# Optimization experiments

Hardware: AMD Instinct MI355X
Metric: run time of the kernel (lower is better)

The kernel has to match this reference:

```python
import jax, jax.numpy as jnp
import numpy as np

NUM_HEAD = 16
D_MODEL = 1024


def setup_inputs() -> dict:
    key = jax.random.key(0)
    ks = jax.random.split(key, 11)
    B, S, D = 2, 2048, D_MODEL
    scale = 1.0 / np.sqrt(D)
    inp = {
        "q": jax.random.normal(ks[0], (B, S, D), dtype=jnp.float32),
        "k": jax.random.normal(ks[1], (B, S, D), dtype=jnp.float32),
        "v": jax.random.normal(ks[2], (B, S, D), dtype=jnp.float32),
        "Wq": jax.random.normal(ks[3], (D, D), dtype=jnp.float32) * scale,
        "bq": jnp.zeros((D,), dtype=jnp.float32),
        "Wk": jax.random.normal(ks[4], (D, D), dtype=jnp.float32) * scale,
        "bk": jnp.zeros((D,), dtype=jnp.float32),
        "Wv": jax.random.normal(ks[5], (D, D), dtype=jnp.float32) * scale,
        "bv": jnp.zeros((D,), dtype=jnp.float32),
        "Wo": jax.random.normal(ks[6], (D, D), dtype=jnp.float32) * scale,
        "bo": jnp.zeros((D,), dtype=jnp.float32),
    }
    return inp


def _split_heads(x, num_head):
    B, S, D = x.shape
    return x.reshape(B, S, num_head, D // num_head).transpose(0, 2, 1, 3)  # [B,H,S,d]


def reference(q, k, v, Wq, bq, Wk, bk, Wv, bv, Wo, bo):
    H = NUM_HEAD
    qp = q @ Wq + bq
    kp = k @ Wk + bk  # computed but UNUSED, matching source bug
    vp = v @ Wv + bv
    # source bug: k := split_heads(v-projection)
    qh = _split_heads(qp, H)          # [B,H,S,d]
    kh = _split_heads(vp, H)          # [B,H,S,d]  (v-projection used as keys)
    vh = _split_heads(vp, H)          # [B,H,S,d]
    d = qh.shape[-1]
    scores = jnp.einsum('bhqd,bhkd->bhqk', qh, kh) / jnp.sqrt(jnp.asarray(d, qh.dtype))
    attn = jax.nn.softmax(scores, axis=-1)
    out = jnp.einsum('bhqk,bhkd->bhqd', attn, vh)  # [B,H,S,d]
    B, _, S, _ = out.shape
    out = out.transpose(0, 2, 1, 3).reshape(B, S, H * d)
    return out @ Wo + bo
```

## Files before the change

### kernel.cpp

```cpp
#include <hip/hip_runtime.h>
#include <hip/hip_bf16.h>

using bfrag  = __attribute__((ext_vector_type(8))) __bf16;
using f32x4  = __attribute__((ext_vector_type(4))) float;
using f32x16 = __attribute__((ext_vector_type(16))) float;
using v4u    = __attribute__((ext_vector_type(4))) unsigned int;
using v2u    = __attribute__((ext_vector_type(2))) unsigned int;

__device__ __forceinline__ ushort f2bf(float f) {
    union { float f; unsigned u; } c; c.f = f;
    return (ushort)((c.u + 0x7fffu + ((c.u >> 16) & 1u)) >> 16);
}

__device__ __forceinline__ unsigned pack_bf16x2(float lo, float hi) {
    union { __hip_bfloat162 h; unsigned u; } c;
    c.h = __float22bfloat162_rn(make_float2(lo, hi));
    return c.u;
}

__device__ __forceinline__ void gld_lds16(const ushort* g, ushort* l) {
    __builtin_amdgcn_global_load_lds(
        (const __attribute__((address_space(1))) void*)g,
        (__attribute__((address_space(3))) void*)l, 16, 0, 0);
}

__device__ __forceinline__ f32x16 mfma32(bfrag a, bfrag b, f32x16 c) {
    return __builtin_amdgcn_mfma_f32_32x32x16_bf16(a, b, c, 0, 0, 0);
}


__global__ void cvt_bf16_2(const float* __restrict__ a, ushort* __restrict__ da,
                           const float* __restrict__ b, ushort* __restrict__ db, int n4) {
    int i = blockIdx.x * blockDim.x + threadIdx.x;
    const float* s; ushort* d;
    if (i < n4) { s = a; d = da; } else { s = b; d = db; i -= n4; }
    float4 f = ((const float4*)s)[i];
    ((ushort4*)d)[i] = make_ushort4(f2bf(f.x), f2bf(f.y), f2bf(f.z), f2bf(f.w));
}

__global__ void cvt_T3(const float* __restrict__ s0, ushort* __restrict__ d0,
                       const float* __restrict__ s1, ushort* __restrict__ d1,
                       const float* __restrict__ s2, ushort* __restrict__ d2) {
    __shared__ float t[32][33];
    const int z = blockIdx.z;
    const float* src = z == 0 ? s0 : z == 1 ? s1 : s2;
    ushort* dst = z == 0 ? d0 : z == 1 ? d1 : d2;
    const int tx = threadIdx.x, ty = threadIdx.y;
    const int c0 = blockIdx.x * 32, r0 = blockIdx.y * 32;
    for (int i = ty; i < 32; i += 8) t[i][tx] = src[(size_t)(r0 + i) * 1024 + c0 + tx];
    __syncthreads();
    for (int i = ty; i < 32; i += 8) dst[(size_t)(c0 + i) * 1024 + r0 + tx] = f2bf(t[tx][i]);
}


__global__ __launch_bounds__(256) void vpt_T(const ushort* __restrict__ VPb, ushort* __restrict__ VPT) {
    __shared__ ushort T[64][72];
    const int st = blockIdx.x, bh = blockIdx.y;
    const int b = bh >> 4, h = bh & 15;
    const int tid = threadIdx.x;
#pragma unroll
    for (int i = 0; i < 2; ++i) {
        const int c = tid + i * 256;
        const int row = c >> 3, col8 = (c & 7) * 8;
        v4u d = *(const v4u*)(VPb + (size_t)(b * 2048 + st * 64 + row) * 1024 + h * 64 + col8);
        *(v4u*)&T[row][col8] = d;
    }
    __syncthreads();
    const int d = tid >> 2, sch = tid & 3;
    union { ushort s[16]; v4u v[2]; } tmp;
#pragma unroll
    for (int j = 0; j < 16; ++j) {
        const int js = (j & 3) | ((j >> 1) & 4) | ((j << 1) & 8);
        tmp.s[j] = T[sch * 16 + js][d];
    }
    ushort* dst = VPT + ((size_t)bh * 64 + d) * 2048 + st * 64 + sch * 16;
    *(v4u*)dst = tmp.v[0];
    *(v4u*)(dst + 8) = tmp.v[1];
}


template<bool BF16OUT>
__device__ __forceinline__ void gemm_body(
    const ushort* __restrict__ A, const ushort* __restrict__ Bt,
    const float* __restrict__ bias, void* __restrict__ Cout,
    float scale, int bM, int bN)
{
    __shared__ ushort As[2][128 * 32];
    __shared__ ushort Bs[2][128 * 32];
    const int tid = threadIdx.x;
    const int lane = tid & 63, w = tid >> 6;
    const int l15 = lane & 15, lg = lane >> 4;
    const int wr = w >> 1, wc = w & 1;

    const ushort* Ag = A + (size_t)bM * 128 * 1024;
    const ushort* Bg = Bt + (size_t)bN * 128 * 1024;
    const int r0 = w * 32 + (lane >> 2);
    const int cc = (lane & 3) * 8;

    auto STAGE = [&](int buf, int kt) {
        const int kk = kt * 32;
#pragma unroll
        for (int i = 0; i < 2; ++i) {
            const int row = r0 + i * 16;
            const int c = w * 2 + i;
            gld_lds16(Ag + (size_t)row * 1024 + kk + cc, &As[buf][c * 512]);
            gld_lds16(Bg + (size_t)row * 1024 + kk + cc, &Bs[buf][c * 512]);
        }
    };

    f32x4 acc[4][4];
#pragma unroll
    for (int m = 0; m < 4; ++m)
#pragma unroll
        for (int n = 0; n < 4; ++n) acc[m][n] = (f32x4){0.f, 0.f, 0.f, 0.f};

    STAGE(0, 0);
    __syncthreads();
    int cur = 0;
    for (int kt = 0; kt < 32; ++kt) {
        if (kt < 31) STAGE(cur ^ 1, kt + 1);
        bfrag aF[4], bF[4];
#pragma unroll
        for (int m = 0; m < 4; ++m) aF[m] = *(const bfrag*)&As[cur][(wr * 64 + m * 16 + l15) * 32 + lg * 8];
#pragma unroll
        for (int n = 0; n < 4; ++n) bF[n] = *(const bfrag*)&Bs[cur][(wc * 64 + n * 16 + l15) * 32 + lg * 8];
        __builtin_amdgcn_s_setprio(1);
#pragma unroll
        for (int m = 0; m < 4; ++m)
#pragma unroll
            for (int n = 0; n < 4; ++n)
                acc[m][n] = __builtin_amdgcn_mfma_f32_16x16x32_bf16(aF[m], bF[n], acc[m][n], 0, 0, 0);
        __builtin_amdgcn_s_setprio(0);
        if (kt < 31) {
            __syncthreads();
            cur ^= 1;
        }
    }

#pragma unroll
    for (int m = 0; m < 4; ++m)
#pragma unroll
        for (int n = 0; n < 4; ++n) {
            const int gcol = bN * 128 + wc * 64 + n * 16 + l15;
            const float bv = bias[gcol];
#pragma unroll
            for (int j = 0; j < 4; ++j) {
                const int grow = bM * 128 + wr * 64 + m * 16 + lg * 4 + j;
                const float val = (acc[m][n][j] + bv) * scale;
                if constexpr (BF16OUT) {
                    ((ushort*)Cout)[(size_t)grow * 1024 + gcol] = f2bf(val);
                } else {
                    ((float*)Cout)[(size_t)grow * 1024 + gcol] = val;
                }
            }
        }
}

__global__ __launch_bounds__(256) void gemm_qv(
    const ushort* __restrict__ Aq, const ushort* __restrict__ Wq, const float* __restrict__ bq, ushort* __restrict__ Cq,
    const ushort* __restrict__ Av, const ushort* __restrict__ Wv, const float* __restrict__ bv, ushort* __restrict__ Cv,
    float qscale)
{
    const int z = blockIdx.z;
    gemm_body<true>(z ? Av : Aq, z ? Wv : Wq, z ? bv : bq, z ? (void*)Cv : (void*)Cq,
                    z ? 1.0f : qscale, blockIdx.y, blockIdx.x);
}

__global__ __launch_bounds__(256) void gemm_o(
    const ushort* __restrict__ A, const ushort* __restrict__ Bt,
    const float* __restrict__ bias, float* __restrict__ Cout)
{
    gemm_body<false>(A, Bt, bias, Cout, 1.0f, blockIdx.y, blockIdx.x);
}


__global__ __launch_bounds__(512, 2) void attn_kernel(
    const ushort* __restrict__ QP, const ushort* __restrict__ VP,
    const ushort* __restrict__ VPT, ushort* __restrict__ AO)
{
    __shared__ ushort Ks[3][4096];
    __shared__ ushort Vs[2][4096];
    const int tid = threadIdx.x;
    const int w = tid >> 6, lane = tid & 63;
    const int l31 = lane & 31, hi = lane >> 5;
    const int bh = blockIdx.x, qt = blockIdx.y;
    const int b = bh >> 4, h = bh & 15;
    const int qrow0 = qt * 256 + w * 32;

    const int r_st = tid >> 3;
    const int sc = ((tid & 7) ^ (r_st & 7)) * 8;
    const ushort* Kg = VP + (size_t)(b * 2048) * 1024 + h * 64 + sc;
    const ushort* Vg = VPT + (size_t)bh * 131072 + (size_t)r_st * 2048 + sc;

    auto STAGE_K = [&](int slot, int kt) {
        gld_lds16(Kg + (size_t)(kt * 64 + r_st) * 1024, &Ks[slot][tid * 8]);
    };
    auto STAGE_V = [&](int slot, int kt) {
        gld_lds16(Vg + kt * 64, &Vs[slot][tid * 8]);
    };

    const ushort* Qp = QP + ((size_t)(b * 2048 + qrow0 + l31)) * 1024 + h * 64 + hi * 8;
    bfrag qB[4];
#pragma unroll
    for (int ds = 0; ds < 4; ++ds) qB[ds] = *(const bfrag*)(Qp + ds * 16);

    f32x16 O0, O1, SA0, SA1, SB0, SB1;
#pragma unroll
    for (int r = 0; r < 16; ++r) { O0[r] = 0.f; O1[r] = 0.f; }
    float lrun = 0.f;

    const int swz = (l31 & 7) << 4;
    const int cA = hi * 16;

    auto QKT = [&](const ushort* Kb_, f32x16& S0, f32x16& S1) {
        bfrag k0f[4], k1f[4];
#pragma unroll
        for (int ds = 0; ds < 4; ++ds) {
            k0f[ds] = *(const bfrag*)&Kb_[(l31 * 128 + ((ds * 32 + cA) ^ swz)) >> 1];
            k1f[ds] = *(const bfrag*)&Kb_[((l31 + 32) * 128 + ((ds * 32 + cA) ^ swz)) >> 1];
        }
#pragma unroll
        for (int r = 0; r < 16; ++r) { S0[r] = -16.0f; S1[r] = -16.0f; }
        __builtin_amdgcn_s_setprio(1);
#pragma unroll
        for (int ds = 0; ds < 4; ++ds) S0 = mfma32(k0f[ds], qB[ds], S0);
#pragma unroll
        for (int ds = 0; ds < 4; ++ds) S1 = mfma32(k1f[ds], qB[ds], S1);
        __builtin_amdgcn_s_setprio(0);
    };

    STAGE_K(0, 0);
    STAGE_K(1, 1);
    STAGE_V(0, 0);
    __syncthreads();
    QKT(Ks[0], SA0, SA1);

    auto STEP = [&](f32x16& Sc0, f32x16& Sc1, f32x16& Sn0, f32x16& Sn1, int t) {
        if (t > 0) __syncthreads();
        if (t + 2 < 32) STAGE_K((t + 2) % 3, t + 2);
        if (t + 1 < 32) {
            STAGE_V((t + 1) & 1, t + 1);
            QKT(Ks[(t + 1) % 3], Sn0, Sn1);
        }

        const ushort* Vb_ = Vs[t & 1];
        bfrag vF0[4], vF1[4];
#pragma unroll
        for (int c = 0; c < 4; ++c) {
            vF0[c] = *(const bfrag*)&Vb_[(l31 * 128 + ((c * 32 + cA) ^ swz)) >> 1];
            vF1[c] = *(const bfrag*)&Vb_[((l31 + 32) * 128 + ((c * 32 + cA) ^ swz)) >> 1];
        }

        float p[32];
#pragma unroll
        for (int r = 0; r < 16; ++r) {
            p[r]      = __builtin_amdgcn_exp2f(Sc0[r]);
            p[16 + r] = __builtin_amdgcn_exp2f(Sc1[r]);
        }
        float s8[8];
#pragma unroll
        for (int i = 0; i < 8; ++i) s8[i] = (p[i] + p[i + 8]) + (p[i + 16] + p[i + 24]);
        lrun += ((s8[0] + s8[1]) + (s8[2] + s8[3])) + ((s8[4] + s8[5]) + (s8[6] + s8[7]));

        bfrag pB[4];
#pragma unroll
        for (int c = 0; c < 4; ++c) {
            union { v4u u; bfrag f; } cv;
#pragma unroll
            for (int wd = 0; wd < 4; ++wd)
                cv.u[wd] = pack_bf16x2(p[8 * c + 2 * wd], p[8 * c + 2 * wd + 1]);
            pB[c] = cv.f;
        }

        __builtin_amdgcn_s_setprio(1);
#pragma unroll
        for (int c = 0; c < 4; ++c) O0 = mfma32(vF0[c], pB[c], O0);
#pragma unroll
        for (int c = 0; c < 4; ++c) O1 = mfma32(vF1[c], pB[c], O1);
        __builtin_amdgcn_s_setprio(0);
    };

#pragma unroll 1
    for (int t2 = 0; t2 < 16; ++t2) {
        STEP(SA0, SA1, SB0, SB1, 2 * t2);
        STEP(SB0, SB1, SA0, SA1, 2 * t2 + 1);
    }

    lrun += __shfl_xor(lrun, 32);
    const float inv = 1.f / lrun;
    ushort* Ao = AO + (size_t)(b * 2048 + qrow0 + l31) * 1024 + h * 64 + hi * 4;
#pragma unroll
    for (int t = 0; t < 2; ++t) {
#pragma unroll
        for (int g = 0; g < 4; ++g) {
            const float e0 = (t ? O1[4 * g + 0] : O0[4 * g + 0]) * inv;
            const float e1 = (t ? O1[4 * g + 1] : O0[4 * g + 1]) * inv;
            const float e2 = (t ? O1[4 * g + 2] : O0[4 * g + 2]) * inv;
            const float e3 = (t ? O1[4 * g + 3] : O0[4 * g + 3]) * inv;
            v2u pk = (v2u){pack_bf16x2(e0, e1), pack_bf16x2(e2, e3)};
            *(v2u*)(Ao + t * 32 + g * 8) = pk;
        }
    }
}


extern "C" void kernel_launch(void* const* d_in, const int* in_sizes, int n_in,
                              void* d_out, int out_size, void* d_ws, size_t ws_size,
                              hipStream_t stream) {
    (void)in_sizes; (void)n_in; (void)out_size; (void)ws_size;
    const float* q  = (const float*)d_in[0];
    const float* v  = (const float*)d_in[2];
    const float* Wq = (const float*)d_in[3];
    const float* bq = (const float*)d_in[4];
    const float* Wv = (const float*)d_in[7];
    const float* bv = (const float*)d_in[8];
    const float* Wo = (const float*)d_in[9];
    const float* bo = (const float*)d_in[10];
    float* out = (float*)d_out;
    char* ws = (char*)d_ws;
    const size_t MB = 1ull << 20;
    ushort* qbf = (ushort*)(ws + 0);
    ushort* vbf = (ushort*)(ws + 8 * MB);
    ushort* WqT = (ushort*)(ws + 16 * MB);
    ushort* WvT = (ushort*)(ws + 18 * MB);
    ushort* WoT = (ushort*)(ws + 20 * MB);
    ushort* QPb = (ushort*)(ws + 22 * MB);
    ushort* VPb = (ushort*)(ws + 30 * MB);
    ushort* VPT = (ushort*)(ws + 38 * MB);
    ushort* AO  = qbf;

    cvt_bf16_2<<<8192, 256, 0, stream>>>(q, qbf, v, vbf, 1048576);
    cvt_T3<<<dim3(32, 32, 3), dim3(32, 8), 0, stream>>>(Wq, WqT, Wv, WvT, Wo, WoT);

    const float qscale = 0.125f * 1.44269504088896340736f;
    gemm_qv<<<dim3(8, 32, 2), 256, 0, stream>>>(qbf, WqT, bq, QPb,
                                                vbf, WvT, bv, VPb, qscale);
    vpt_T<<<dim3(32, 32), 256, 0, stream>>>(VPb, VPT);
    attn_kernel<<<dim3(32, 8), 512, 0, stream>>>(QPb, VPb, VPT, AO);
    gemm_o<<<dim3(8, 32), 256, 0, stream>>>(AO, WoT, bo, out);
}
```

Baseline: 131.4 us.

## Split attention over key halves with 64 query rows per wave and combine kernel

Each wave now processes 64 query rows instead of 32, so every K/V fragment loaded from LDS feeds twice as many MFMAs. The key range is split into two halves across blockIdx.z, which keeps the grid at 256 blocks. Partial outputs (bf16) and row sums are written to workspace, and a new combine kernel adds and normalizes them. This adds an extra kernel launch, extra global traffic for the partials, bf16 rounding of the partials, higher register pressure, and removes the triple-buffered K pipeline that overlapped QK^T with PV.

```diff
diff --git a/kernel.cpp b/kernel.cpp
--- a/kernel.cpp
+++ b/kernel.cpp
@@ -10,6 +10,10 @@
 __device__ __forceinline__ ushort f2bf(float f) {
     union { float f; unsigned u; } c; c.f = f;
     return (ushort)((c.u + 0x7fffu + ((c.u >> 16) & 1u)) >> 16);
+}
+
+__device__ __forceinline__ float bf2f(ushort u) {
+    union { unsigned u; float f; } c; c.u = (unsigned)u << 16; return c.f;
 }
 
 __device__ __forceinline__ unsigned pack_bf16x2(float lo, float hi) {
@@ -176,131 +180,164 @@
 
 __global__ __launch_bounds__(512, 2) void attn_kernel(
     const ushort* __restrict__ QP, const ushort* __restrict__ VP,
-    const ushort* __restrict__ VPT, ushort* __restrict__ AO)
-{
-    __shared__ ushort Ks[3][4096];
+    const ushort* __restrict__ VPT, ushort* __restrict__ Opart, float* __restrict__ Lpart)
+{
+    __shared__ ushort Ks[2][4096];
     __shared__ ushort Vs[2][4096];
     const int tid = threadIdx.x;
     const int w = tid >> 6, lane = tid & 63;
     const int l31 = lane & 31, hi = lane >> 5;
-    const int bh = blockIdx.x, qt = blockIdx.y;
+    const int bh = blockIdx.x, qt = blockIdx.y, half = blockIdx.z;
     const int b = bh >> 4, h = bh & 15;
-    const int qrow0 = qt * 256 + w * 32;
+    const int qrow0 = qt * 512 + w * 64;
+    const int k0 = half * 16;
 
     const int r_st = tid >> 3;
     const int sc = ((tid & 7) ^ (r_st & 7)) * 8;
     const ushort* Kg = VP + (size_t)(b * 2048) * 1024 + h * 64 + sc;
     const ushort* Vg = VPT + (size_t)bh * 131072 + (size_t)r_st * 2048 + sc;
 
-    auto STAGE_K = [&](int slot, int kt) {
+    auto STAGE = [&](int slot, int kt) {
         gld_lds16(Kg + (size_t)(kt * 64 + r_st) * 1024, &Ks[slot][tid * 8]);
-    };
-    auto STAGE_V = [&](int slot, int kt) {
         gld_lds16(Vg + kt * 64, &Vs[slot][tid * 8]);
     };
 
     const ushort* Qp = QP + ((size_t)(b * 2048 + qrow0 + l31)) * 1024 + h * 64 + hi * 8;
-    bfrag qB[4];
-#pragma unroll
-    for (int ds = 0; ds < 4; ++ds) qB[ds] = *(const bfrag*)(Qp + ds * 16);
-
-    f32x16 O0, O1, SA0, SA1, SB0, SB1;
-#pragma unroll
-    for (int r = 0; r < 16; ++r) { O0[r] = 0.f; O1[r] = 0.f; }
-    float lrun = 0.f;
+    bfrag qA[4], qBt[4];
+#pragma unroll
+    for (int ds = 0; ds < 4; ++ds) {
+        qA[ds]  = *(const bfrag*)(Qp + ds * 16);
+        qBt[ds] = *(const bfrag*)(Qp + 32 * 1024 + ds * 16);
+    }
+
+    f32x16 OA0, OA1, OB0, OB1;
+#pragma unroll
+    for (int r = 0; r < 16; ++r) { OA0[r] = 0.f; OA1[r] = 0.f; OB0[r] = 0.f; OB1[r] = 0.f; }
+    float lrunA = 0.f, lrunB = 0.f;
 
     const int swz = (l31 & 7) << 4;
     const int cA = hi * 16;
 
-    auto QKT = [&](const ushort* Kb_, f32x16& S0, f32x16& S1) {
+    STAGE(0, k0);
+    __syncthreads();
+
+    auto SOFTMAX = [&](f32x16& S0, f32x16& S1, bfrag (&pB)[4], float& lrun) {
+        float p[32];
+#pragma unroll
+        for (int r = 0; r < 16; ++r) {
+            p[r]      = __builtin_amdgcn_exp2f(S0[r]);
+            p[16 + r] = __builtin_amdgcn_exp2f(S1[r]);
+        }
+        float s8[8];
+#pragma unroll
+        for (int i = 0; i < 8; ++i) s8[i] = (p[i] + p[i + 8]) + (p[i + 16] + p[i + 24]);
+        lrun += ((s8[0] + s8[1]) + (s8[2] + s8[3])) + ((s8[4] + s8[5]) + (s8[6] + s8[7]));
+#pragma unroll
+        for (int c = 0; c < 4; ++c) {
+            union { v4u u; bfrag f; } cv;
+#pragma unroll
+            for (int wd = 0; wd < 4; ++wd)
+                cv.u[wd] = pack_bf16x2(p[8 * c + 2 * wd], p[8 * c + 2 * wd + 1]);
+            pB[c] = cv.f;
+        }
+    };
+
+#pragma unroll 1
+    for (int t = 0; t < 16; ++t) {
+        if (t > 0) __syncthreads();
+        if (t + 1 < 16) STAGE((t + 1) & 1, k0 + t + 1);
+        const ushort* Kb_ = Ks[t & 1];
+        const ushort* Vb_ = Vs[t & 1];
+
         bfrag k0f[4], k1f[4];
 #pragma unroll
         for (int ds = 0; ds < 4; ++ds) {
             k0f[ds] = *(const bfrag*)&Kb_[(l31 * 128 + ((ds * 32 + cA) ^ swz)) >> 1];
             k1f[ds] = *(const bfrag*)&Kb_[((l31 + 32) * 128 + ((ds * 32 + cA) ^ swz)) >> 1];
         }
-#pragma unroll
-        for (int r = 0; r < 16; ++r) { S0[r] = -16.0f; S1[r] = -16.0f; }
+        f32x16 SA0, SA1, SB0, SB1;
+#pragma unroll
+        for (int r = 0; r < 16; ++r) { SA0[r] = -16.f; SA1[r] = -16.f; SB0[r] = -16.f; SB1[r] = -16.f; }
         __builtin_amdgcn_s_setprio(1);
 #pragma unroll
-        for (int ds = 0; ds < 4; ++ds) S0 = mfma32(k0f[ds], qB[ds], S0);
-#pragma unroll
-        for (int ds = 0; ds < 4; ++ds) S1 = mfma32(k1f[ds], qB[ds], S1);
+        for (int ds = 0; ds < 4; ++ds) {
+            SA0 = mfma32(k0f[ds], qA[ds], SA0);
+            SA1 = mfma32(k1f[ds], qA[ds], SA1);
+            SB0 = mfma32(k0f[ds], qBt[ds], SB0);
+            SB1 = mfma32(k1f[ds], qBt[ds], SB1);
+        }
         __builtin_amdgcn_s_setprio(0);
-    };
-
-    STAGE_K(0, 0);
-    STAGE_K(1, 1);
-    STAGE_V(0, 0);
-    __syncthreads();
-    QKT(Ks[0], SA0, SA1);
-
-    auto STEP = [&](f32x16& Sc0, f32x16& Sc1, f32x16& Sn0, f32x16& Sn1, int t) {
-        if (t > 0) __syncthreads();
-        if (t + 2 < 32) STAGE_K((t + 2) % 3, t + 2);
-        if (t + 1 < 32) {
-            STAGE_V((t + 1) & 1, t + 1);
-            QKT(Ks[(t + 1) % 3], Sn0, Sn1);
-        }
-
-        const ushort* Vb_ = Vs[t & 1];
+
+        bfrag pBA[4], pBB[4];
+        SOFTMAX(SA0, SA1, pBA, lrunA);
+        SOFTMAX(SB0, SB1, pBB, lrunB);
+
         bfrag vF0[4], vF1[4];
 #pragma unroll
         for (int c = 0; c < 4; ++c) {
             vF0[c] = *(const bfrag*)&Vb_[(l31 * 128 + ((c * 32 + cA) ^ swz)) >> 1];
             vF1[c] = *(const bfrag*)&Vb_[((l31 + 32) * 128 + ((c * 32 + cA) ^ swz)) >> 1];
         }
-
-        float p[32];
-#pragma unroll
-        for (int r = 0; r < 16; ++r) {
-            p[r]      = __builtin_amdgcn_exp2f(Sc0[r]);
-            p[16 + r] = __builtin_amdgcn_exp2f(Sc1[r]);
-        }
-        float s8[8];
-#pragma unroll
-        for (int i = 0; i < 8; ++i) s8[i] = (p[i] + p[i + 8]) + (p[i + 16] + p[i + 24]);
-        lrun += ((s8[0] + s8[1]) + (s8[2] + s8[3])) + ((s8[4] + s8[5]) + (s8[6] + s8[7]));
-
-        bfrag pB[4];
+        __builtin_amdgcn_s_setprio(1);
 #pragma unroll
         for (int c = 0; c < 4; ++c) {
-            union { v4u u; bfrag f; } cv;
-#pragma unroll
-            for (int wd = 0; wd < 4; ++wd)
-                cv.u[wd] = pack_bf16x2(p[8 * c + 2 * wd], p[8 * c + 2 * wd + 1]);
-            pB[c] = cv.f;
-        }
-
-        __builtin_amdgcn_s_setprio(1);
-#pragma unroll
-        for (int c = 0; c < 4; ++c) O0 = mfma32(vF0[c], pB[c], O0);
-#pragma unroll
-        for (int c = 0; c < 4; ++c) O1 = mfma32(vF1[c], pB[c], O1);
+            OA0 = mfma32(vF0[c], pBA[c], OA0);
+            OA1 = mfma32(vF1[c], pBA[c], OA1);
+            OB0 = mfma32(vF0[c], pBB[c], OB0);
+            OB1 = mfma32(vF1[c], pBB[c], OB1);
+        }
         __builtin_amdgcn_s_setprio(0);
-    };
-
-#pragma unroll 1
-    for (int t2 = 0; t2 < 16; ++t2) {
-        STEP(SA0, SA1, SB0, SB1, 2 * t2);
-        STEP(SB0, SB1, SA0, SA1, 2 * t2 + 1);
-    }
-
-    lrun += __shfl_xor(lrun, 32);
-    const float inv = 1.f / lrun;
-    ushort* Ao = AO + (size_t)(b * 2048 + qrow0 + l31) * 1024 + h * 64 + hi * 4;
+    }
+
+    lrunA += __shfl_xor(lrunA, 32);
+    lrunB += __shfl_xor(lrunB, 32);
+    ushort* AoA = Opart + (size_t)half * 4194304
+                + (size_t)(b * 2048 + qrow0 + l31) * 1024 + h * 64 + hi * 4;
+    ushort* AoB = AoA + 32 * 1024;
 #pragma unroll
     for (int t = 0; t < 2; ++t) {
 #pragma unroll
         for (int g = 0; g < 4; ++g) {
-            const float e0 = (t ? O1[4 * g + 0] : O0[4 * g + 0]) * inv;
-            const float e1 = (t ? O1[4 * g + 1] : O0[4 * g + 1]) * inv;
-            const float e2 = (t ? O1[4 * g + 2] : O0[4 * g + 2]) * inv;
-            const float e3 = (t ? O1[4 * g + 3] : O0[4 * g + 3]) * inv;
-            v2u pk = (v2u){pack_bf16x2(e0, e1), pack_bf16x2(e2, e3)};
-            *(v2u*)(Ao + t * 32 + g * 8) = pk;
-        }
-    }
+            const float a0 = t ? OA1[4 * g + 0] : OA0[4 * g + 0];
+            const float a1 = t ? OA1[4 * g + 1] : OA0[4 * g + 1];
+            const float a2 = t ? OA1[4 * g + 2] : OA0[4 * g + 2];
+            const float a3 = t ? OA1[4 * g + 3] : OA0[4 * g + 3];
+            *(v2u*)(AoA + t * 32 + g * 8) = (v2u){pack_bf16x2(a0, a1), pack_bf16x2(a2, a3)};
+            const float b0 = t ? OB1[4 * g + 0] : OB0[4 * g + 0];
+            const float b1 = t ? OB1[4 * g + 1] : OB0[4 * g + 1];
+            const float b2 = t ? OB1[4 * g + 2] : OB0[4 * g + 2];
+            const float b3 = t ? OB1[4 * g + 3] : OB0[4 * g + 3];
+            *(v2u*)(AoB + t * 32 + g * 8) = (v2u){pack_bf16x2(b0, b1), pack_bf16x2(b2, b3)};
+        }
+    }
+    if (hi == 0) {
+        Lpart[half * 65536 + bh * 2048 + qrow0 + l31] = lrunA;
+        Lpart[half * 65536 + bh * 2048 + qrow0 + 32 + l31] = lrunB;
+    }
+}
+
+
+__global__ __launch_bounds__(256) void combine_kernel(
+    const ushort* __restrict__ Opart, const float* __restrict__ Lpart,
+    ushort* __restrict__ AO)
+{
+    const int t = blockIdx.x * 256 + threadIdx.x;
+    const int e0 = t * 8;
+    const int grow = e0 >> 10, col = e0 & 1023;
+    const int b = grow >> 11, s = grow & 2047, h = col >> 6;
+    const int li = (b * 16 + h) * 2048 + s;
+    const float l = Lpart[li] + Lpart[65536 + li];
+    const float inv = 1.0f / l;
+    v4u a = *(const v4u*)(Opart + e0);
+    v4u c = *(const v4u*)(Opart + 4194304 + e0);
+    v4u o;
+#pragma unroll
+    for (int wd = 0; wd < 4; ++wd) {
+        const float x0 = (bf2f((ushort)(a[wd] & 0xffff)) + bf2f((ushort)(c[wd] & 0xffff))) * inv;
+        const float x1 = (bf2f((ushort)(a[wd] >> 16))    + bf2f((ushort)(c[wd] >> 16)))    * inv;
+        o[wd] = pack_bf16x2(x0, x1);
+    }
+    *(v4u*)(AO + e0) = o;
 }
 
 
@@ -327,7 +364,10 @@
     ushort* QPb = (ushort*)(ws + 22 * MB);
     ushort* VPb = (ushort*)(ws + 30 * MB);
     ushort* VPT = (ushort*)(ws + 38 * MB);
-    ushort* AO  = qbf;
+
+    ushort* Opart = (ushort*)(ws + 0);
+    float*  Lpart = (float*)(ws + 16 * MB);
+    ushort* AO    = QPb;
 
     cvt_bf16_2<<<8192, 256, 0, stream>>>(q, qbf, v, vbf, 1048576);
     cvt_T3<<<dim3(32, 32, 3), dim3(32, 8), 0, stream>>>(Wq, WqT, Wv, WvT, Wo, WoT);
@@ -336,6 +376,7 @@
     gemm_qv<<<dim3(8, 32, 2), 256, 0, stream>>>(qbf, WqT, bq, QPb,
                                                 vbf, WvT, bv, VPb, qscale);
     vpt_T<<<dim3(32, 32), 256, 0, stream>>>(VPb, VPT);
-    attn_kernel<<<dim3(32, 8), 512, 0, stream>>>(QPb, VPb, VPT, AO);
+    attn_kernel<<<dim3(32, 4, 2), 512, 0, stream>>>(QPb, VPb, VPT, Opart, Lpart);
+    combine_kernel<<<2048, 256, 0, stream>>>(Opart, Lpart, AO);
     gemm_o<<<dim3(8, 32), 256, 0, stream>>>(AO, WoT, bo, out);
 }
```

Measured after the change: 133.2 us. Within noise of the previous version (+1.4%).
